# Kernel tuning notes

Hardware: AMD Instinct MI355X
Metric: run time of the kernel (lower is better)

## Reference

```python
import jax, jax.numpy as jnp
import numpy as np

LOG2 = 0.6931471805599453

def ssp(x):
    # ShiftedSoftplus: softplus(x) - log(2)
    return jax.nn.softplus(x) - jnp.asarray(LOG2, x.dtype)

def setup_inputs() -> dict:
    key = jax.random.key(0)
    ks = jax.random.split(key, 12)
    B, N, D, F, R, P = 1, 50000, 128, 128, 20, 1600000
    s = lambda fan_in: 1.0 / np.sqrt(fan_in)
    return {
        "x": jax.random.normal(ks[0], (B, N, D), jnp.float32),
        "f_ij": jax.random.uniform(ks[1], (P, R), jnp.float32),
        "idx_i": jax.random.randint(ks[2], (P,), 0, B * N),
        "idx_j": jax.random.randint(ks[3], (P,), 0, B * N),
        "rcut_ij": jax.random.uniform(ks[4], (P,), jnp.float32),
        "W_in": jax.random.uniform(ks[5], (F, D), jnp.float32, -s(D), s(D)),
        "b_in": jax.random.uniform(ks[6], (F,), jnp.float32, -s(D), s(D)),
        "W_filter": jax.random.uniform(ks[7], (F, R), jnp.float32, -s(R), s(R)),
        "b_filter": jax.random.uniform(ks[8], (F,), jnp.float32, -s(R), s(R)),
        "W_out": jax.random.uniform(ks[9], (D, F), jnp.float32, -s(F), s(F)),
        "b_out": jax.random.uniform(ks[10], (D,), jnp.float32, -s(F), s(F)),
    }

def reference(x, f_ij, idx_i, idx_j, rcut_ij, W_in, b_in, W_filter, b_filter, W_out, b_out):
    B, N, _ = x.shape
    # input_to_feature: Linear(nr_atom_basis -> nr_filters)
    h = jnp.einsum('bnd,fd->bnf', x, W_in) + b_in          # [B,N,F]
    h = h.reshape(B * N, -1)                                # [B*N,F]
    # filter network: Linear(nr_rbf -> nr_filters) + ShiftedSoftplus, scaled by cutoff
    Wij = ssp(jnp.einsum('pr,fr->pf', f_ij, W_filter) + b_filter) * rcut_ij[:, None]  # [P,F]
    # gather -> mul -> scatter_add
    x_ij = h[idx_j] * Wij                                   # [P,F]
    agg = jax.ops.segment_sum(x_ij, idx_i, num_segments=B * N)  # [B*N,F]
    # feature_to_output: Linear(nr_filters -> nr_atom_basis) + ShiftedSoftplus
    out = ssp(jnp.einsum('nf,df->nd', agg, W_out) + b_out)  # [B*N,D]
    return out.reshape(B, N, 128)
```

## Files before the change

### kernel.cpp

```cpp
#include <hip/hip_runtime.h>
#include <hip/hip_bf16.h>

static constexpr float kLog2 = 0.6931471805599453f;

__device__ __forceinline__ float sspf(float x) {
    return fmaxf(x, 0.0f) + __logf(1.0f + __expf(-fabsf(x))) - kLog2;
}

typedef __attribute__((ext_vector_type(8))) _Float16 half8;
typedef __attribute__((ext_vector_type(4))) _Float16 half4v;
typedef __attribute__((ext_vector_type(4))) float float4v;

template <bool ACT, typename OUT>
__device__ __forceinline__ void gemm_mfma_body(const float* __restrict__ A,
                                               const float* __restrict__ B,
                                               const float* __restrict__ bias,
                                               OUT* __restrict__ C, int M,
                                               int blockid) {
    constexpr int LDH = 136;
    __shared__ _Float16 Als[64 * LDH];
    __shared__ _Float16 Bls[128 * LDH];
    const int tid = threadIdx.x;
    const int rowbase = blockid * 64;
#pragma unroll
    for (int j = 0; j < 8; ++j) {
        int idx = j * 256 + tid;
        int r = idx >> 5, c4 = (idx & 31) << 2;
        int rg = rowbase + r;
        rg = rg < M ? rg : (M - 1);
        float4 v = *(const float4*)(A + (size_t)rg * 128 + c4);
        half4v hv = {(_Float16)v.x, (_Float16)v.y, (_Float16)v.z, (_Float16)v.w};
        *(half4v*)&Als[r * LDH + c4] = hv;
    }
#pragma unroll
    for (int j = 0; j < 16; ++j) {
        int idx = j * 256 + tid;
        int r = idx >> 5, c4 = (idx & 31) << 2;
        float4 v = *(const float4*)(B + (size_t)r * 128 + c4);
        half4v hv = {(_Float16)v.x, (_Float16)v.y, (_Float16)v.z, (_Float16)v.w};
        *(half4v*)&Bls[r * LDH + c4] = hv;
    }
    __syncthreads();

    const int wave = tid >> 6, lane = tid & 63;
    const int l15 = lane & 15, q = lane >> 4;
    float4v acc[8];
#pragma unroll
    for (int nt = 0; nt < 8; ++nt) acc[nt] = (float4v){0.f, 0.f, 0.f, 0.f};
    const int am = wave * 16 + l15;
#pragma unroll
    for (int kk = 0; kk < 4; ++kk) {
        half8 af = *(const half8*)&Als[am * LDH + kk * 32 + q * 8];
#pragma unroll
        for (int nt = 0; nt < 8; ++nt) {
            half8 bfv = *(const half8*)&Bls[(nt * 16 + l15) * LDH + kk * 32 + q * 8];
            acc[nt] = __builtin_amdgcn_mfma_f32_16x16x32_f16(af, bfv, acc[nt], 0, 0, 0);
        }
    }
#pragma unroll
    for (int nt = 0; nt < 8; ++nt) {
        int n = nt * 16 + l15;
        float bv = bias[n];
#pragma unroll
        for (int r = 0; r < 4; ++r) {
            int m = rowbase + wave * 16 + q * 4 + r;
            if (m < M) {
                float v = acc[nt][r] + bv;
                if (ACT) v = sspf(v);
                C[(size_t)m * 128 + n] = (OUT)v;
            }
        }
    }
}

__global__ __launch_bounds__(256) void gemm_in_count_kernel(
    const float* __restrict__ A, const float* __restrict__ B,
    const float* __restrict__ bias, _Float16* __restrict__ C, int M,
    const int* __restrict__ idx_i, int* __restrict__ counts, int P,
    int gemm_blocks) {
    if ((int)blockIdx.x < gemm_blocks) {
        gemm_mfma_body<false, _Float16>(A, B, bias, C, M, blockIdx.x);
    } else {
        const int nthr = (gridDim.x - gemm_blocks) * 256;
        for (int p = (blockIdx.x - gemm_blocks) * 256 + threadIdx.x; p < P;
             p += nthr)
            atomicAdd(&counts[idx_i[p]], 1);
    }
}

__global__ __launch_bounds__(256) void gemm_out_kernel(
    const float* __restrict__ A, const float* __restrict__ B,
    const float* __restrict__ bias, float* __restrict__ C, int M) {
    gemm_mfma_body<true, float>(A, B, bias, C, M, blockIdx.x);
}

__global__ __launch_bounds__(256) void alloc_starts_kernel(
    const int* __restrict__ counts, int* __restrict__ starts,
    int* __restrict__ cursor, int* __restrict__ gtot, int N) {
    __shared__ int s[256];
    __shared__ int base;
    const int t = threadIdx.x, g = blockIdx.x * 256 + t;
    const int c = g < N ? counts[g] : 0;
    s[t] = c;
    __syncthreads();
    for (int o = 1; o < 256; o <<= 1) {
        int v = t >= o ? s[t - o] : 0;
        __syncthreads();
        s[t] += v;
        __syncthreads();
    }
    if (t == 255) base = atomicAdd(gtot, s[255]);
    __syncthreads();
    const int excl = base + s[t] - c;
    if (g < N) {
        starts[g] = excl;
        cursor[g] = excl;
    }
}

template <bool EF>
__global__ __launch_bounds__(256) void fill_kernel(
    const int* __restrict__ idx_i, const int* __restrict__ idx_j,
    const float* __restrict__ rcut, const float* __restrict__ f_ij,
    int* __restrict__ cursor, _Float16* __restrict__ ef,
    int2* __restrict__ meta, int* __restrict__ pidx, int P) {
    int p = blockIdx.x * 256 + threadIdx.x;
    if (p >= P) return;
    const int i = idx_i[p];
    const int pos = atomicAdd(&cursor[i], 1);
    meta[pos] = make_int2(idx_j[p] << 7, __float_as_int(rcut[p]));
    if (EF) {
        const float* fr = f_ij + (size_t)p * 20;
        _Float16 hb[24];
#pragma unroll
        for (int r = 0; r < 20; r += 4) {
            float4 v = *(const float4*)(fr + r);
            hb[r] = (_Float16)v.x; hb[r + 1] = (_Float16)v.y;
            hb[r + 2] = (_Float16)v.z; hb[r + 3] = (_Float16)v.w;
        }
        hb[20] = (_Float16)1.0f; hb[21] = (_Float16)0.0f;
        hb[22] = (_Float16)0.0f; hb[23] = (_Float16)0.0f;
        _Float16* dst = ef + (size_t)pos * 24;
        *(half8*)dst = *(half8*)hb;
        *(half8*)(dst + 8) = *(half8*)(hb + 8);
        *(half8*)(dst + 16) = *(half8*)(hb + 16);
    } else {
        pidx[pos] = p;
    }
}

template <bool EF>
__global__ __launch_bounds__(256, 4) void gather_mfma_kernel(
    const _Float16* __restrict__ ef, const int2* __restrict__ meta,
    const int* __restrict__ pidx, const float* __restrict__ f_ij,
    const float* __restrict__ Wf, const float* __restrict__ bf,
    const _Float16* __restrict__ h16, const int* __restrict__ starts,
    const int* __restrict__ counts, float* __restrict__ agg, int N) {
    const int lane = threadIdx.x & 63;
    const int gwave = (blockIdx.x * 256 + threadIdx.x) >> 6;
    const int nwaves = (gridDim.x * 256) >> 6;
    const int l15 = lane & 15, q = lane >> 4;
    const int fh = gwave & 1;
    const int fbase = fh * 64;

    half8 wfr[4];
#pragma unroll
    for (int t = 0; t < 4; ++t) {
        const int n = fbase + t * 16 + l15;
        const float* wr = Wf + (size_t)n * 20;
        float v[8];
#pragma unroll
        for (int j = 0; j < 8; ++j) {
            int k = q * 8 + j;
            v[j] = (k < 20) ? wr[k] : ((k == 20) ? bf[n] : 0.0f);
        }
        wfr[t] = (half8){(_Float16)v[0], (_Float16)v[1], (_Float16)v[2],
                         (_Float16)v[3], (_Float16)v[4], (_Float16)v[5],
                         (_Float16)v[6], (_Float16)v[7]};
    }
    const float4v zero = {0.f, 0.f, 0.f, 0.f};
    const _Float16* hbase = h16 + fbase + q * 4;

    for (int u = gwave; u < 2 * N; u += nwaves) {
        const int i = u >> 1;
        const int s = __builtin_amdgcn_readfirstlane(starts[i]);
        const int cnt = __builtin_amdgcn_readfirstlane(counts[i]);
        const int e = s + cnt;
        float4v acc[4];
#pragma unroll
        for (int t = 0; t < 4; ++t) acc[t] = zero;

        if (cnt > 0) {
            int pos0 = min(s + l15, e - 1);
            int2 mt_c = meta[pos0];
            half8 bf_c = {};
            int p_c = 0;
            if (EF) {
                if (q < 3) bf_c = *(const half8*)(ef + (size_t)pos0 * 24 + q * 8);
            } else {
                p_c = pidx[pos0];
            }
            int2 mt_n = mt_c;
            half8 bf_n = bf_c;
            int p_n = p_c;
            if (s + 16 < e) {
                int pos1 = min(s + 16 + l15, e - 1);
                mt_n = meta[pos1];
                if (EF) {
                    if (q < 3) bf_n = *(const half8*)(ef + (size_t)pos1 * 24 + q * 8);
                } else {
                    p_n = pidx[pos1];
                }
            }
            half4v hv_c[4];
            {
                const _Float16* hp = hbase + mt_c.x;
#pragma unroll
                for (int t = 0; t < 4; ++t) hv_c[t] = *(const half4v*)(hp + t * 16);
            }

            for (int c = s; c < e; c += 16) {
                half4v hv_n[4];
                if (c + 16 < e) {
                    const _Float16* hp = hbase + mt_n.x;
#pragma unroll
                    for (int t = 0; t < 4; ++t) hv_n[t] = *(const half4v*)(hp + t * 16);
                }
                int2 mt_n2 = mt_n;
                half8 bf_n2 = bf_n;
                int p_n2 = p_n;
                if (c + 32 < e) {
                    int pos2 = min(c + 32 + l15, e - 1);
                    mt_n2 = meta[pos2];
                    if (EF) {
                        if (q < 3) bf_n2 = *(const half8*)(ef + (size_t)pos2 * 24 + q * 8);
                    } else {
                        p_n2 = pidx[pos2];
                    }
                }
                if (!EF) {
                    const float* fp = f_ij + (size_t)p_c * 20;
                    float b0 = 0.f, b1 = 0.f, b2 = 0.f, b3 = 0.f;
                    float b4 = 0.f, b5 = 0.f, b6 = 0.f, b7 = 0.f;
                    if (q <= 2) {
                        float4 a = *(const float4*)(fp + q * 8);
                        b0 = a.x; b1 = a.y; b2 = a.z; b3 = a.w;
                    }
                    if (q <= 1) {
                        float4 bb = *(const float4*)(fp + q * 8 + 4);
                        b4 = bb.x; b5 = bb.y; b6 = bb.z; b7 = bb.w;
                    }
                    if (q == 2) b4 = 1.0f;
                    bf_c = (half8){(_Float16)b0, (_Float16)b1, (_Float16)b2,
                                   (_Float16)b3, (_Float16)b4, (_Float16)b5,
                                   (_Float16)b6, (_Float16)b7};
                }
                const float rc = (c + l15 < e) ? __int_as_float(mt_c.y) : 0.0f;
#pragma unroll
                for (int t = 0; t < 4; ++t) {
                    float4v d = __builtin_amdgcn_mfma_f32_16x16x32_f16(
                        wfr[t], bf_c, zero, 0, 0, 0);
#pragma unroll
                    for (int r = 0; r < 4; ++r) {
                        float w = sspf(d[r]) * rc;
                        acc[t][r] = fmaf(w, (float)hv_c[t][r], acc[t][r]);
                    }
                }
                mt_c = mt_n; mt_n = mt_n2;
                bf_c = bf_n; bf_n = bf_n2;
                p_c = p_n;   p_n = p_n2;
#pragma unroll
                for (int t = 0; t < 4; ++t) hv_c[t] = hv_n[t];
            }
        }
#pragma unroll
        for (int m = 1; m <= 8; m <<= 1)
#pragma unroll
            for (int t = 0; t < 4; ++t)
#pragma unroll
                for (int r = 0; r < 4; ++r)
                    acc[t][r] += __shfl_xor(acc[t][r], m, 64);
        if (l15 == 0) {
#pragma unroll
            for (int t = 0; t < 4; ++t) {
                float4 o = {acc[t][0], acc[t][1], acc[t][2], acc[t][3]};
                *(float4*)(agg + (size_t)i * 128 + fbase + t * 16 + q * 4) = o;
            }
        }
    }
}

extern "C" void kernel_launch(void* const* d_in, const int* in_sizes, int n_in,
                              void* d_out, int out_size, void* d_ws, size_t ws_size,
                              hipStream_t stream) {
    const float* x     = (const float*)d_in[0];
    const float* f_ij  = (const float*)d_in[1];
    const int*   idx_i = (const int*)d_in[2];
    const int*   idx_j = (const int*)d_in[3];
    const float* rcut  = (const float*)d_in[4];
    const float* W_in  = (const float*)d_in[5];
    const float* b_in  = (const float*)d_in[6];
    const float* W_f   = (const float*)d_in[7];
    const float* b_f   = (const float*)d_in[8];
    const float* W_out = (const float*)d_in[9];
    const float* b_out = (const float*)d_in[10];

    const int N = in_sizes[0] / 128;
    const int P = in_sizes[2];

    char* ws = (char*)d_ws;
    size_t off = 0;
    auto alloc = [&](size_t bytes) {
        void* ptr = ws + off;
        off += (bytes + 15) & ~(size_t)15;
        return ptr;
    };
    int* counts  = (int*)alloc((size_t)N * 4 + 16);
    int* gtot    = counts + N;
    int* starts  = (int*)alloc((size_t)N * 4);
    int* cursor  = (int*)alloc((size_t)N * 4);
    _Float16* h16 = (_Float16*)alloc((size_t)N * 128 * 2);
    int2* meta   = (int2*)alloc((size_t)P * 8);
    size_t base_need = off;
    const bool use_ef = (base_need + (size_t)P * 24 * 2 + 64) <= ws_size;
    _Float16* ef = nullptr;
    int* pidx = nullptr;
    if (use_ef) ef = (_Float16*)alloc((size_t)P * 24 * 2 + 64);
    else        pidx = (int*)alloc((size_t)P * 4);

    float* agg = (float*)d_out;

    const int mblocks = (N + 63) / 64;
    const int cblocks = 768;
    const int NB = (N + 255) / 256;

    hipMemsetAsync(counts, 0, (size_t)N * 4 + 16, stream);
    gemm_in_count_kernel<<<mblocks + cblocks, 256, 0, stream>>>(
        x, W_in, b_in, h16, N, idx_i, counts, P, mblocks);
    alloc_starts_kernel<<<NB, 256, 0, stream>>>(counts, starts, cursor, gtot, N);
    if (use_ef) {
        fill_kernel<true><<<(P + 255) / 256, 256, 0, stream>>>(
            idx_i, idx_j, rcut, f_ij, cursor, ef, meta, pidx, P);
        gather_mfma_kernel<true><<<4096, 256, 0, stream>>>(
            ef, meta, pidx, f_ij, W_f, b_f, h16, starts, counts, agg, N);
    } else {
        fill_kernel<false><<<(P + 255) / 256, 256, 0, stream>>>(
            idx_i, idx_j, rcut, f_ij, cursor, ef, meta, pidx, P);
        gather_mfma_kernel<false><<<4096, 256, 0, stream>>>(
            ef, meta, pidx, f_ij, W_f, b_f, h16, starts, counts, agg, N);
    }
    gemm_out_kernel<<<mblocks, 256, 0, stream>>>(agg, W_out, b_out, (float*)d_out, N);
}
```

Measured before the change: 627.3 us.

## Precompute filter weights into CSR-ordered fp16 buffer, then lean gather-accumulate

Adds a filter_fill kernel that runs the filter MFMA and shifted softplus once per pair and writes fp16 W_ij rows into CSR order. A lean gather kernel then only loads W_ij and permuted h16 rows and accumulates them, instead of recomputing the filter inside the gather. Depending on workspace size, the filter is split into 1, 2 or 4 column chunks of 128/64/32 features. This removes MFMA and transcendental work from the latency-bound gather. In exchange it writes and re-reads a P×128 fp16 buffer, roughly 400 MB of extra traffic, and adds launches in the low-workspace modes.

```diff
diff --git a/kernel.cpp b/kernel.cpp
--- a/kernel.cpp
+++ b/kernel.cpp
@@ -11,7 +11,7 @@
 typedef __attribute__((ext_vector_type(4))) _Float16 half4v;
 typedef __attribute__((ext_vector_type(4))) float float4v;
 
-template <bool ACT, typename OUT>
+template <bool PERM, bool ACT, typename OUT>
 __device__ __forceinline__ void gemm_mfma_body(const float* __restrict__ A,
                                                const float* __restrict__ B,
                                                const float* __restrict__ bias,
@@ -61,25 +61,31 @@
     for (int nt = 0; nt < 8; ++nt) {
         int n = nt * 16 + l15;
         float bv = bias[n];
+        int pn = n;
+        if (PERM) {
+            pn = ((n >> 6) << 6) + (((n >> 2) & 3) << 4) + (((n >> 4) & 3) << 2) +
+                 (n & 3);
+        }
 #pragma unroll
         for (int r = 0; r < 4; ++r) {
             int m = rowbase + wave * 16 + q * 4 + r;
             if (m < M) {
                 float v = acc[nt][r] + bv;
                 if (ACT) v = sspf(v);
-                C[(size_t)m * 128 + n] = (OUT)v;
-            }
-        }
-    }
-}
-
+                C[(size_t)m * 128 + pn] = (OUT)v;
+            }
+        }
+    }
+}
+
+template <bool PERM>
 __global__ __launch_bounds__(256) void gemm_in_count_kernel(
     const float* __restrict__ A, const float* __restrict__ B,
     const float* __restrict__ bias, _Float16* __restrict__ C, int M,
     const int* __restrict__ idx_i, int* __restrict__ counts, int P,
     int gemm_blocks) {
     if ((int)blockIdx.x < gemm_blocks) {
-        gemm_mfma_body<false, _Float16>(A, B, bias, C, M, blockIdx.x);
+        gemm_mfma_body<PERM, false, _Float16>(A, B, bias, C, M, blockIdx.x);
     } else {
         const int nthr = (gridDim.x - gemm_blocks) * 256;
         for (int p = (blockIdx.x - gemm_blocks) * 256 + threadIdx.x; p < P;
@@ -91,7 +97,7 @@
 __global__ __launch_bounds__(256) void gemm_out_kernel(
     const float* __restrict__ A, const float* __restrict__ B,
     const float* __restrict__ bias, float* __restrict__ C, int M) {
-    gemm_mfma_body<true, float>(A, B, bias, C, M, blockIdx.x);
+    gemm_mfma_body<false, true, float>(A, B, bias, C, M, blockIdx.x);
 }
 
 __global__ __launch_bounds__(256) void alloc_starts_kernel(
@@ -115,6 +121,212 @@
     if (g < N) {
         starts[g] = excl;
         cursor[g] = excl;
+    }
+}
+
+
+template <int FT, bool ASSIGN>
+__global__ __launch_bounds__(256) void filter_fill_kernel(
+    const float* __restrict__ f_ij, const int* __restrict__ idx_i,
+    const int* __restrict__ idx_j, const float* __restrict__ rcut,
+    const float* __restrict__ Wf, const float* __restrict__ bfil,
+    int* __restrict__ cursor, int* __restrict__ meta, int* __restrict__ posof,
+    _Float16* __restrict__ wij, int P, int stride, int fb) {
+    const int lane = threadIdx.x & 63;
+    const int gw = (blockIdx.x * 256 + threadIdx.x) >> 6;
+    const int pb = gw * 16;
+    if (pb >= P) return;
+    const int l15 = lane & 15, q = lane >> 4;
+
+    half8 wfr[FT];
+#pragma unroll
+    for (int t = 0; t < FT; ++t) {
+        const int n = fb + t * 16 + l15;
+        const float* wr = Wf + (size_t)n * 20;
+        float v[8];
+#pragma unroll
+        for (int j = 0; j < 8; ++j) {
+            int k = q * 8 + j;
+            v[j] = (k < 20) ? wr[k] : ((k == 20) ? bfil[n] : 0.0f);
+        }
+        wfr[t] = (half8){(_Float16)v[0], (_Float16)v[1], (_Float16)v[2],
+                         (_Float16)v[3], (_Float16)v[4], (_Float16)v[5],
+                         (_Float16)v[6], (_Float16)v[7]};
+    }
+
+    const int p = pb + l15;
+    const bool pv = p < P;
+    const int pc = pv ? p : (P - 1);
+    const float rc = rcut[pc];
+
+    int pos;
+    if (ASSIGN) {
+        int pos0 = 0;
+        if (q == 0 && pv) {
+            pos0 = atomicAdd(&cursor[idx_i[p]], 1);
+            meta[pos0] = idx_j[p] << 7;
+            posof[p] = pos0;
+        }
+        pos = __shfl(pos0, l15, 64);
+    } else {
+        pos = posof[pc];
+    }
+
+    const float* fp = f_ij + (size_t)pc * 20;
+    float b0 = 0.f, b1 = 0.f, b2 = 0.f, b3 = 0.f;
+    float b4 = 0.f, b5 = 0.f, b6 = 0.f, b7 = 0.f;
+    if (q <= 2) {
+        float4 a = *(const float4*)(fp + q * 8);
+        b0 = a.x; b1 = a.y; b2 = a.z; b3 = a.w;
+    }
+    if (q <= 1) {
+        float4 bb = *(const float4*)(fp + q * 8 + 4);
+        b4 = bb.x; b5 = bb.y; b6 = bb.z; b7 = bb.w;
+    }
+    if (q == 2) b4 = 1.0f;
+    const half8 bfc = (half8){(_Float16)b0, (_Float16)b1, (_Float16)b2,
+                              (_Float16)b3, (_Float16)b4, (_Float16)b5,
+                              (_Float16)b6, (_Float16)b7};
+
+    const float4v zero = {0.f, 0.f, 0.f, 0.f};
+    const float rcln2 = rc * 0.69314718f;
+    _Float16 wst[FT * 4];
+#pragma unroll
+    for (int t = 0; t < FT; ++t) {
+        float4v d = __builtin_amdgcn_mfma_f32_16x16x32_f16(wfr[t], bfc, zero, 0, 0, 0);
+#pragma unroll
+        for (int r = 0; r < 4; ++r) {
+            float x = d[r];
+            float mx = fmaxf(x, 0.0f);
+            float e2 = exp2f(-fabsf(x) * 1.44269504f);
+            float lg = log2f(1.0f + e2);
+            float w = fmaf(lg, rcln2, fmaf(mx, rc, -rcln2));
+            wst[t * 4 + r] = (_Float16)w;
+        }
+    }
+    if (pv) {
+        _Float16* wb = wij + (size_t)pos * stride;
+        if (FT == 8) {
+            *(half8*)(wb + q * 16) = *(half8*)&wst[0];
+            *(half8*)(wb + q * 16 + 8) = *(half8*)&wst[8];
+            *(half8*)(wb + 64 + q * 16) = *(half8*)&wst[16];
+            *(half8*)(wb + 64 + q * 16 + 8) = *(half8*)&wst[24];
+        } else if (FT == 4) {
+            *(half8*)(wb + q * 16) = *(half8*)&wst[0];
+            *(half8*)(wb + q * 16 + 8) = *(half8*)&wst[8];
+        } else {
+            *(half8*)(wb + q * 8) = *(half8*)&wst[0];
+        }
+    }
+}
+
+template <int GT>
+__global__ __launch_bounds__(256) void gather_lean_kernel(
+    const _Float16* __restrict__ wij, const int* __restrict__ meta,
+    const _Float16* __restrict__ h16, const int* __restrict__ starts,
+    const int* __restrict__ counts, float* __restrict__ agg, int units,
+    int stride, int fb_fixed, int split) {
+    constexpr int NH = GT / 2;
+    const int lane = threadIdx.x & 63;
+    const int gwave = (blockIdx.x * 256 + threadIdx.x) >> 6;
+    const int nwaves = (gridDim.x * 256) >> 6;
+    const int l15 = lane & 15, q = lane >> 4;
+    const half8 hzero = {};
+
+    for (int u = gwave; u < units; u += nwaves) {
+        int i, fbw, woff;
+        if (split) {
+            i = u >> 1;
+            fbw = (u & 1) << 6;
+            woff = fbw + (q << 4);
+        } else {
+            i = u;
+            fbw = fb_fixed;
+            woff = q * (GT * 4);
+        }
+        const int hoff = ((fbw >> 6) << 6) + (q << 4) + (((fbw >> 4) & 3) << 2);
+        const int s = __builtin_amdgcn_readfirstlane(starts[i]);
+        const int cnt = __builtin_amdgcn_readfirstlane(counts[i]);
+        const int e = s + cnt;
+        float4v acc[GT];
+#pragma unroll
+        for (int t = 0; t < GT; ++t) acc[t] = (float4v){0.f, 0.f, 0.f, 0.f};
+
+        if (cnt > 0) {
+            int pos_c = min(s + l15, e - 1);
+            bool vl_c = (s + l15) < e;
+            int jb_c = meta[pos_c];
+            half8 wv_c[NH], hv_c[NH];
+            {
+                const _Float16* wp = wij + (size_t)pos_c * stride + woff;
+                const _Float16* hp = h16 + jb_c + hoff;
+#pragma unroll
+                for (int h = 0; h < NH; ++h) {
+                    wv_c[h] = *(const half8*)(wp + h * 8);
+                    hv_c[h] = *(const half8*)(hp + h * 8);
+                }
+            }
+            int pos_n = pos_c, jb_n = jb_c;
+            bool vl_n = false;
+            if (s + 16 < e) {
+                pos_n = min(s + 16 + l15, e - 1);
+                jb_n = meta[pos_n];
+                vl_n = (s + 16 + l15) < e;
+            }
+            for (int c = s; c < e; c += 16) {
+                half8 wv_n[NH], hv_n[NH];
+                if (c + 16 < e) {
+                    const _Float16* wp = wij + (size_t)pos_n * stride + woff;
+                    const _Float16* hp = h16 + jb_n + hoff;
+#pragma unroll
+                    for (int h = 0; h < NH; ++h) {
+                        wv_n[h] = *(const half8*)(wp + h * 8);
+                        hv_n[h] = *(const half8*)(hp + h * 8);
+                    }
+                }
+                int pos_n2 = pos_n, jb_n2 = jb_n;
+                bool vl_n2 = vl_n;
+                if (c + 32 < e) {
+                    pos_n2 = min(c + 32 + l15, e - 1);
+                    jb_n2 = meta[pos_n2];
+                    vl_n2 = (c + 32 + l15) < e;
+                }
+                if (!vl_c) {
+#pragma unroll
+                    for (int h = 0; h < NH; ++h) wv_c[h] = hzero;
+                }
+#pragma unroll
+                for (int h = 0; h < NH; ++h) {
+#pragma unroll
+                    for (int j = 0; j < 8; ++j) {
+                        int t = (h * 8 + j) >> 2, r = j & 3;
+                        acc[t][r] = fmaf((float)wv_c[h][j], (float)hv_c[h][j],
+                                         acc[t][r]);
+                    }
+                }
+#pragma unroll
+                for (int h = 0; h < NH; ++h) {
+                    wv_c[h] = wv_n[h];
+                    hv_c[h] = hv_n[h];
+                }
+                vl_c = vl_n; vl_n = vl_n2;
+                pos_n = pos_n2; jb_n = jb_n2;
+            }
+        }
+#pragma unroll
+        for (int m = 1; m <= 8; m <<= 1)
+#pragma unroll
+            for (int t = 0; t < GT; ++t)
+#pragma unroll
+                for (int r = 0; r < 4; ++r)
+                    acc[t][r] += __shfl_xor(acc[t][r], m, 64);
+        if (l15 == 0) {
+#pragma unroll
+            for (int t = 0; t < GT; ++t) {
+                float4 o = {acc[t][0], acc[t][1], acc[t][2], acc[t][3]};
+                *(float4*)(agg + (size_t)i * 128 + fbw + t * 16 + q * 4) = o;
+            }
+        }
     }
 }
 
@@ -255,6 +467,8 @@
                                    (_Float16)b3, (_Float16)b4, (_Float16)b5,
                                    (_Float16)b6, (_Float16)b7};
                 }
+                const int jb = mt_c.x;
+                (void)jb;
                 const float rc = (c + l15 < e) ? __int_as_float(mt_c.y) : 0.0f;
 #pragma unroll
                 for (int t = 0; t < 4; ++t) {
@@ -308,6 +522,24 @@
     const int N = in_sizes[0] / 128;
     const int P = in_sizes[2];
 
+    const int mblocks = (N + 63) / 64;
+    const int cblocks = 768;
+    const int NB = (N + 255) / 256;
+    float* agg = (float*)d_out;
+
+    auto pad16 = [](size_t b) { return (b + 15) & ~(size_t)15; };
+
+    size_t base_new = pad16((size_t)N * 4 + 16) + pad16((size_t)N * 4) +
+                      pad16((size_t)N * 4) + pad16((size_t)N * 128 * 2) +
+                      pad16((size_t)P * 4) + pad16((size_t)P * 4);
+    auto wij_bytes = [&](int stride) { return pad16((size_t)P * stride * 2 + 64); };
+
+    int mode;
+    if (base_new + wij_bytes(128) <= ws_size) mode = 0;
+    else if (base_new + wij_bytes(64) <= ws_size) mode = 1;
+    else if (base_new + wij_bytes(32) <= ws_size) mode = 2;
+    else mode = 3;
+
     char* ws = (char*)d_ws;
     size_t off = 0;
     auto alloc = [&](size_t bytes) {
@@ -315,12 +547,74 @@
         off += (bytes + 15) & ~(size_t)15;
         return ptr;
     };
+
+    if (mode != 3) {
+        int* counts  = (int*)alloc((size_t)N * 4 + 16);
+        int* gtot    = counts + N;
+        int* starts  = (int*)alloc((size_t)N * 4);
+        int* cursor  = (int*)alloc((size_t)N * 4);
+        _Float16* h16 = (_Float16*)alloc((size_t)N * 128 * 2);
+        int* meta    = (int*)alloc((size_t)P * 4);
+        int* posof   = (int*)alloc((size_t)P * 4);
+        const int stride = (mode == 0) ? 128 : (mode == 1 ? 64 : 32);
+        _Float16* wij = (_Float16*)alloc((size_t)P * stride * 2 + 64);
+
+        hipMemsetAsync(counts, 0, (size_t)N * 4 + 16, stream);
+        gemm_in_count_kernel<true><<<mblocks + cblocks, 256, 0, stream>>>(
+            x, W_in, b_in, h16, N, idx_i, counts, P, mblocks);
+        alloc_starts_kernel<<<NB, 256, 0, stream>>>(counts, starts, cursor, gtot, N);
+
+        const int fblocks = (P + 63) / 64;
+        if (mode == 0) {
+            filter_fill_kernel<8, true><<<fblocks, 256, 0, stream>>>(
+                f_ij, idx_i, idx_j, rcut, W_f, b_f, cursor, meta, posof, wij, P,
+                128, 0);
+            gather_lean_kernel<4><<<4096, 256, 0, stream>>>(
+                wij, meta, h16, starts, counts, agg, 2 * N, 128, 0, 1);
+        } else if (mode == 1) {
+            filter_fill_kernel<4, true><<<fblocks, 256, 0, stream>>>(
+                f_ij, idx_i, idx_j, rcut, W_f, b_f, cursor, meta, posof, wij, P,
+                64, 0);
+            gather_lean_kernel<4><<<4096, 256, 0, stream>>>(
+                wij, meta, h16, starts, counts, agg, N, 64, 0, 0);
+            filter_fill_kernel<4, false><<<fblocks, 256, 0, stream>>>(
+                f_ij, idx_i, idx_j, rcut, W_f, b_f, cursor, meta, posof, wij, P,
+                64, 64);
+            gather_lean_kernel<4><<<4096, 256, 0, stream>>>(
+                wij, meta, h16, starts, counts, agg, N, 64, 64, 0);
+        } else {
+            filter_fill_kernel<2, true><<<fblocks, 256, 0, stream>>>(
+                f_ij, idx_i, idx_j, rcut, W_f, b_f, cursor, meta, posof, wij, P,
+                32, 0);
+            gather_lean_kernel<2><<<4096, 256, 0, stream>>>(
+                wij, meta, h16, starts, counts, agg, N, 32, 0, 0);
+            filter_fill_kernel<2, false><<<fblocks, 256, 0, stream>>>(
+                f_ij, idx_i, idx_j, rcut, W_f, b_f, cursor, meta, posof, wij, P,
+                32, 32);
+            gather_lean_kernel<2><<<4096, 256, 0, stream>>>(
+                wij, meta, h16, starts, counts, agg, N, 32, 32, 0);
+            filter_fill_kernel<2, false><<<fblocks, 256, 0, stream>>>(
+                f_ij, idx_i, idx_j, rcut, W_f, b_f, cursor, meta, posof, wij, P,
+                32, 64);
+            gather_lean_kernel<2><<<4096, 256, 0, stream>>>(
+                wij, meta, h16, starts, counts, agg, N, 32, 64, 0);
+            filter_fill_kernel<2, false><<<fblocks, 256, 0, stream>>>(
+                f_ij, idx_i, idx_j, rcut, W_f, b_f, cursor, meta, posof, wij, P,
+                32, 96);
+            gather_lean_kernel<2><<<4096, 256, 0, stream>>>(
+                wij, meta, h16, starts, counts, agg, N, 32, 96, 0);
+        }
+        gemm_out_kernel<<<mblocks, 256, 0, stream>>>(agg, W_out, b_out,
+                                                     (float*)d_out, N);
+        return;
+    }
+
     int* counts  = (int*)alloc((size_t)N * 4 + 16);
     int* gtot    = counts + N;
     int* starts  = (int*)alloc((size_t)N * 4);
     int* cursor  = (int*)alloc((size_t)N * 4);
     _Float16* h16 = (_Float16*)alloc((size_t)N * 128 * 2);
-    int2* meta   = (int2*)alloc((size_t)P * 8);
+    int2* meta2  = (int2*)alloc((size_t)P * 8);
     size_t base_need = off;
     const bool use_ef = (base_need + (size_t)P * 24 * 2 + 64) <= ws_size;
     _Float16* ef = nullptr;
@@ -328,26 +622,20 @@
     if (use_ef) ef = (_Float16*)alloc((size_t)P * 24 * 2 + 64);
     else        pidx = (int*)alloc((size_t)P * 4);
 
-    float* agg = (float*)d_out;
-
-    const int mblocks = (N + 63) / 64;
-    const int cblocks = 768;
-    const int NB = (N + 255) / 256;
-
     hipMemsetAsync(counts, 0, (size_t)N * 4 + 16, stream);
-    gemm_in_count_kernel<<<mblocks + cblocks, 256, 0, stream>>>(
+    gemm_in_count_kernel<false><<<mblocks + cblocks, 256, 0, stream>>>(
         x, W_in, b_in, h16, N, idx_i, counts, P, mblocks);
     alloc_starts_kernel<<<NB, 256, 0, stream>>>(counts, starts, cursor, gtot, N);
     if (use_ef) {
         fill_kernel<true><<<(P + 255) / 256, 256, 0, stream>>>(
-            idx_i, idx_j, rcut, f_ij, cursor, ef, meta, pidx, P);
+            idx_i, idx_j, rcut, f_ij, cursor, ef, meta2, pidx, P);
         gather_mfma_kernel<true><<<4096, 256, 0, stream>>>(
-            ef, meta, pidx, f_ij, W_f, b_f, h16, starts, counts, agg, N);
+            ef, meta2, pidx, f_ij, W_f, b_f, h16, starts, counts, agg, N);
     } else {
         fill_kernel<false><<<(P + 255) / 256, 256, 0, stream>>>(
-            idx_i, idx_j, rcut, f_ij, cursor, ef, meta, pidx, P);
+            idx_i, idx_j, rcut, f_ij, cursor, ef, meta2, pidx, P);
         gather_mfma_kernel<false><<<4096, 256, 0, stream>>>(
-            ef, meta, pidx, f_ij, W_f, b_f, h16, starts, counts, agg, N);
+            ef, meta2, pidx, f_ij, W_f, b_f, h16, starts, counts, agg, N);
     }
     gemm_out_kernel<<<mblocks, 256, 0, stream>>>(agg, W_out, b_out, (float*)d_out, N);
 }
```

New measurement: 1.023 ms. +63.1%, slower.

## Permute h16 columns so one wave gathers full 128-feature rows per atom

Applied to the files above, without the earlier changes.

The input GEMM now writes h16 with a permuted column order, so each lane can load contiguous half8 chunks that match the MFMA output layout of the filter network. The gather kernel processes all 128 filters per atom in a single wave instead of splitting them across two waves. This halves the metadata and edge-feature loads and the filter MFMA input setup per edge. In exchange it doubles the register footprint (8 filter fragments, 8 accumulators), so the occupancy hint of 4 is removed and occupancy and latency hiding may drop.

```diff
diff --git a/kernel.cpp b/kernel.cpp
--- a/kernel.cpp
+++ b/kernel.cpp
@@ -11,7 +11,12 @@
 typedef __attribute__((ext_vector_type(4))) _Float16 half4v;
 typedef __attribute__((ext_vector_type(4))) float float4v;
 
-template <bool ACT, typename OUT>
+__device__ __forceinline__ int hperm(int n) {
+    return ((n >> 6) << 6) | (((n >> 5) & 1) << 5) | (((n >> 2) & 3) << 3) |
+           (((n >> 4) & 1) << 2) | (n & 3);
+}
+
+template <bool PERM, bool ACT, typename OUT>
 __device__ __forceinline__ void gemm_mfma_body(const float* __restrict__ A,
                                                const float* __restrict__ B,
                                                const float* __restrict__ bias,
@@ -61,13 +66,14 @@
     for (int nt = 0; nt < 8; ++nt) {
         int n = nt * 16 + l15;
         float bv = bias[n];
+        const int pn = PERM ? hperm(n) : n;
 #pragma unroll
         for (int r = 0; r < 4; ++r) {
             int m = rowbase + wave * 16 + q * 4 + r;
             if (m < M) {
                 float v = acc[nt][r] + bv;
                 if (ACT) v = sspf(v);
-                C[(size_t)m * 128 + n] = (OUT)v;
+                C[(size_t)m * 128 + pn] = (OUT)v;
             }
         }
     }
@@ -79,7 +85,7 @@
     const int* __restrict__ idx_i, int* __restrict__ counts, int P,
     int gemm_blocks) {
     if ((int)blockIdx.x < gemm_blocks) {
-        gemm_mfma_body<false, _Float16>(A, B, bias, C, M, blockIdx.x);
+        gemm_mfma_body<true, false, _Float16>(A, B, bias, C, M, blockIdx.x);
     } else {
         const int nthr = (gridDim.x - gemm_blocks) * 256;
         for (int p = (blockIdx.x - gemm_blocks) * 256 + threadIdx.x; p < P;
@@ -91,7 +97,7 @@
 __global__ __launch_bounds__(256) void gemm_out_kernel(
     const float* __restrict__ A, const float* __restrict__ B,
     const float* __restrict__ bias, float* __restrict__ C, int M) {
-    gemm_mfma_body<true, float>(A, B, bias, C, M, blockIdx.x);
+    gemm_mfma_body<false, true, float>(A, B, bias, C, M, blockIdx.x);
 }
 
 __global__ __launch_bounds__(256) void alloc_starts_kernel(
@@ -150,7 +156,7 @@
 }
 
 template <bool EF>
-__global__ __launch_bounds__(256, 4) void gather_mfma_kernel(
+__global__ __launch_bounds__(256) void gather_mfma_kernel(
     const _Float16* __restrict__ ef, const int2* __restrict__ meta,
     const int* __restrict__ pidx, const float* __restrict__ f_ij,
     const float* __restrict__ Wf, const float* __restrict__ bf,
@@ -160,35 +166,30 @@
     const int gwave = (blockIdx.x * 256 + threadIdx.x) >> 6;
     const int nwaves = (gridDim.x * 256) >> 6;
     const int l15 = lane & 15, q = lane >> 4;
-    const int fh = gwave & 1;
-    const int fbase = fh * 64;
-
-    half8 wfr[4];
-#pragma unroll
-    for (int t = 0; t < 4; ++t) {
-        const int n = fbase + t * 16 + l15;
-        const float* wr = Wf + (size_t)n * 20;
+
+    half8 wfr[8];
+#pragma unroll
+    for (int t = 0; t < 8; ++t) {
+        const float* wr = Wf + (size_t)(t * 16 + l15) * 20;
         float v[8];
 #pragma unroll
         for (int j = 0; j < 8; ++j) {
             int k = q * 8 + j;
-            v[j] = (k < 20) ? wr[k] : ((k == 20) ? bf[n] : 0.0f);
+            v[j] = (k < 20) ? wr[k] : ((k == 20) ? bf[t * 16 + l15] : 0.0f);
         }
         wfr[t] = (half8){(_Float16)v[0], (_Float16)v[1], (_Float16)v[2],
                          (_Float16)v[3], (_Float16)v[4], (_Float16)v[5],
                          (_Float16)v[6], (_Float16)v[7]};
     }
     const float4v zero = {0.f, 0.f, 0.f, 0.f};
-    const _Float16* hbase = h16 + fbase + q * 4;
-
-    for (int u = gwave; u < 2 * N; u += nwaves) {
-        const int i = u >> 1;
+
+    for (int i = gwave; i < N; i += nwaves) {
         const int s = __builtin_amdgcn_readfirstlane(starts[i]);
         const int cnt = __builtin_amdgcn_readfirstlane(counts[i]);
         const int e = s + cnt;
-        float4v acc[4];
-#pragma unroll
-        for (int t = 0; t < 4; ++t) acc[t] = zero;
+        float4v acc[8];
+#pragma unroll
+        for (int t = 0; t < 8; ++t) acc[t] = zero;
 
         if (cnt > 0) {
             int pos0 = min(s + l15, e - 1);
@@ -212,25 +213,27 @@
                     p_n = pidx[pos1];
                 }
             }
-            half4v hv_c[4];
+            half8 hv_c[4];
             {
-                const _Float16* hp = hbase + mt_c.x;
-#pragma unroll
-                for (int t = 0; t < 4; ++t) hv_c[t] = *(const half4v*)(hp + t * 16);
-            }
-
-            for (int c = s; c < e; c += 16) {
-                half4v hv_n[4];
-                if (c + 16 < e) {
-                    const _Float16* hp = hbase + mt_n.x;
-#pragma unroll
-                    for (int t = 0; t < 4; ++t) hv_n[t] = *(const half4v*)(hp + t * 16);
+                const _Float16* hp = h16 + mt_c.x + q * 8;
+#pragma unroll
+                for (int c4 = 0; c4 < 4; ++c4)
+                    hv_c[c4] = *(const half8*)(hp + c4 * 32);
+            }
+
+            for (int c0 = s; c0 < e; c0 += 16) {
+                half8 hv_n[4];
+                if (c0 + 16 < e) {
+                    const _Float16* hp = h16 + mt_n.x + q * 8;
+#pragma unroll
+                    for (int c4 = 0; c4 < 4; ++c4)
+                        hv_n[c4] = *(const half8*)(hp + c4 * 32);
                 }
                 int2 mt_n2 = mt_n;
                 half8 bf_n2 = bf_n;
                 int p_n2 = p_n;
-                if (c + 32 < e) {
-                    int pos2 = min(c + 32 + l15, e - 1);
+                if (c0 + 32 < e) {
+                    int pos2 = min(c0 + 32 + l15, e - 1);
                     mt_n2 = meta[pos2];
                     if (EF) {
                         if (q < 3) bf_n2 = *(const half8*)(ef + (size_t)pos2 * 24 + q * 8);
@@ -255,36 +258,37 @@
                                    (_Float16)b3, (_Float16)b4, (_Float16)b5,
                                    (_Float16)b6, (_Float16)b7};
                 }
-                const float rc = (c + l15 < e) ? __int_as_float(mt_c.y) : 0.0f;
-#pragma unroll
-                for (int t = 0; t < 4; ++t) {
+                const float rc = (c0 + l15 < e) ? __int_as_float(mt_c.y) : 0.0f;
+#pragma unroll
+                for (int t = 0; t < 8; ++t) {
                     float4v d = __builtin_amdgcn_mfma_f32_16x16x32_f16(
                         wfr[t], bf_c, zero, 0, 0, 0);
+                    const int hc = t >> 1, hb = (t & 1) * 4;
 #pragma unroll
                     for (int r = 0; r < 4; ++r) {
                         float w = sspf(d[r]) * rc;
-                        acc[t][r] = fmaf(w, (float)hv_c[t][r], acc[t][r]);
+                        acc[t][r] = fmaf(w, (float)hv_c[hc][hb + r], acc[t][r]);
                     }
                 }
                 mt_c = mt_n; mt_n = mt_n2;
                 bf_c = bf_n; bf_n = bf_n2;
                 p_c = p_n;   p_n = p_n2;
 #pragma unroll
-                for (int t = 0; t < 4; ++t) hv_c[t] = hv_n[t];
+                for (int c4 = 0; c4 < 4; ++c4) hv_c[c4] = hv_n[c4];
             }
         }
 #pragma unroll
         for (int m = 1; m <= 8; m <<= 1)
 #pragma unroll
-            for (int t = 0; t < 4; ++t)
+            for (int t = 0; t < 8; ++t)
 #pragma unroll
                 for (int r = 0; r < 4; ++r)
                     acc[t][r] += __shfl_xor(acc[t][r], m, 64);
         if (l15 == 0) {
 #pragma unroll
-            for (int t = 0; t < 4; ++t) {
+            for (int t = 0; t < 8; ++t) {
                 float4 o = {acc[t][0], acc[t][1], acc[t][2], acc[t][3]};
-                *(float4*)(agg + (size_t)i * 128 + fbase + t * 16 + q * 4) = o;
+                *(float4*)(agg + (size_t)i * 128 + t * 16 + q * 4) = o;
             }
         }
     }
```

Result: slower. 695.2 us (+10.8%).

## Drop packed fp16 edge-feature buffer; gather f_ij directly and permute h16 columns

Applied to the files above, without the earlier changes.

The fill kernel no longer converts and scatters f_ij into a sorted fp16 buffer. It only writes a 16-byte meta record (idx_j offset, rcut, original edge index). The gather kernel reads f_ij rows directly through the stored edge index, prefetching one chunk ahead. The input GEMM writes h16 with a column permutation so each lane loads two half8 vectors instead of four half4 vectors. This removes the 1.6M×48-byte ef write and read in exchange for random reads of f_ij in the gather and a larger meta record, and it drops the h prefetch pipelining.

```diff
diff --git a/kernel.cpp b/kernel.cpp
--- a/kernel.cpp
+++ b/kernel.cpp
@@ -11,7 +11,12 @@
 typedef __attribute__((ext_vector_type(4))) _Float16 half4v;
 typedef __attribute__((ext_vector_type(4))) float float4v;
 
-template <bool ACT, typename OUT>
+__device__ __forceinline__ int hperm(int n) {
+    return ((n >> 6) << 6) | (((n >> 5) & 1) << 5) | (((n >> 2) & 3) << 3) |
+           (((n >> 4) & 1) << 2) | (n & 3);
+}
+
+template <bool PERM, bool ACT, typename OUT>
 __device__ __forceinline__ void gemm_mfma_body(const float* __restrict__ A,
                                                const float* __restrict__ B,
                                                const float* __restrict__ bias,
@@ -61,13 +66,14 @@
     for (int nt = 0; nt < 8; ++nt) {
         int n = nt * 16 + l15;
         float bv = bias[n];
+        const int pn = PERM ? hperm(n) : n;
 #pragma unroll
         for (int r = 0; r < 4; ++r) {
             int m = rowbase + wave * 16 + q * 4 + r;
             if (m < M) {
                 float v = acc[nt][r] + bv;
                 if (ACT) v = sspf(v);
-                C[(size_t)m * 128 + n] = (OUT)v;
+                C[(size_t)m * 128 + pn] = (OUT)v;
             }
         }
     }
@@ -79,7 +85,7 @@
     const int* __restrict__ idx_i, int* __restrict__ counts, int P,
     int gemm_blocks) {
     if ((int)blockIdx.x < gemm_blocks) {
-        gemm_mfma_body<false, _Float16>(A, B, bias, C, M, blockIdx.x);
+        gemm_mfma_body<true, false, _Float16>(A, B, bias, C, M, blockIdx.x);
     } else {
         const int nthr = (gridDim.x - gemm_blocks) * 256;
         for (int p = (blockIdx.x - gemm_blocks) * 256 + threadIdx.x; p < P;
@@ -91,7 +97,7 @@
 __global__ __launch_bounds__(256) void gemm_out_kernel(
     const float* __restrict__ A, const float* __restrict__ B,
     const float* __restrict__ bias, float* __restrict__ C, int M) {
-    gemm_mfma_body<true, float>(A, B, bias, C, M, blockIdx.x);
+    gemm_mfma_body<false, true, float>(A, B, bias, C, M, blockIdx.x);
 }
 
 __global__ __launch_bounds__(256) void alloc_starts_kernel(
@@ -118,41 +124,18 @@
     }
 }
 
-template <bool EF>
-__global__ __launch_bounds__(256) void fill_kernel(
+__global__ __launch_bounds__(256) void fill16_kernel(
     const int* __restrict__ idx_i, const int* __restrict__ idx_j,
-    const float* __restrict__ rcut, const float* __restrict__ f_ij,
-    int* __restrict__ cursor, _Float16* __restrict__ ef,
-    int2* __restrict__ meta, int* __restrict__ pidx, int P) {
+    const float* __restrict__ rcut, int* __restrict__ cursor,
+    int4* __restrict__ meta, int P) {
     int p = blockIdx.x * 256 + threadIdx.x;
     if (p >= P) return;
-    const int i = idx_i[p];
-    const int pos = atomicAdd(&cursor[i], 1);
-    meta[pos] = make_int2(idx_j[p] << 7, __float_as_int(rcut[p]));
-    if (EF) {
-        const float* fr = f_ij + (size_t)p * 20;
-        _Float16 hb[24];
-#pragma unroll
-        for (int r = 0; r < 20; r += 4) {
-            float4 v = *(const float4*)(fr + r);
-            hb[r] = (_Float16)v.x; hb[r + 1] = (_Float16)v.y;
-            hb[r + 2] = (_Float16)v.z; hb[r + 3] = (_Float16)v.w;
-        }
-        hb[20] = (_Float16)1.0f; hb[21] = (_Float16)0.0f;
-        hb[22] = (_Float16)0.0f; hb[23] = (_Float16)0.0f;
-        _Float16* dst = ef + (size_t)pos * 24;
-        *(half8*)dst = *(half8*)hb;
-        *(half8*)(dst + 8) = *(half8*)(hb + 8);
-        *(half8*)(dst + 16) = *(half8*)(hb + 16);
-    } else {
-        pidx[pos] = p;
-    }
-}
-
-template <bool EF>
-__global__ __launch_bounds__(256, 4) void gather_mfma_kernel(
-    const _Float16* __restrict__ ef, const int2* __restrict__ meta,
-    const int* __restrict__ pidx, const float* __restrict__ f_ij,
+    const int pos = atomicAdd(&cursor[idx_i[p]], 1);
+    meta[pos] = make_int4(idx_j[p] << 7, __float_as_int(rcut[p]), p, 0);
+}
+
+__global__ __launch_bounds__(256) void gather_direct_kernel(
+    const int4* __restrict__ meta, const float* __restrict__ f_ij,
     const float* __restrict__ Wf, const float* __restrict__ bf,
     const _Float16* __restrict__ h16, const int* __restrict__ starts,
     const int* __restrict__ counts, float* __restrict__ agg, int N) {
@@ -179,7 +162,7 @@
                          (_Float16)v[6], (_Float16)v[7]};
     }
     const float4v zero = {0.f, 0.f, 0.f, 0.f};
-    const _Float16* hbase = h16 + fbase + q * 4;
+    const _Float16* hws = h16 + fbase + q * 8;
 
     for (int u = gwave; u < 2 * N; u += nwaves) {
         const int i = u >> 1;
@@ -191,86 +174,53 @@
         for (int t = 0; t < 4; ++t) acc[t] = zero;
 
         if (cnt > 0) {
-            int pos0 = min(s + l15, e - 1);
-            int2 mt_c = meta[pos0];
-            half8 bf_c = {};
-            int p_c = 0;
-            if (EF) {
-                if (q < 3) bf_c = *(const half8*)(ef + (size_t)pos0 * 24 + q * 8);
-            } else {
-                p_c = pidx[pos0];
-            }
-            int2 mt_n = mt_c;
-            half8 bf_n = bf_c;
-            int p_n = p_c;
-            if (s + 16 < e) {
-                int pos1 = min(s + 16 + l15, e - 1);
-                mt_n = meta[pos1];
-                if (EF) {
-                    if (q < 3) bf_n = *(const half8*)(ef + (size_t)pos1 * 24 + q * 8);
-                } else {
-                    p_n = pidx[pos1];
-                }
-            }
-            half4v hv_c[4];
+            int4 mt_c = meta[min(s + l15, e - 1)];
+            int4 mt_n = (s + 16 < e) ? meta[min(s + 16 + l15, e - 1)] : mt_c;
+            float4 fa_c = {0, 0, 0, 0}, fb_c = {0, 0, 0, 0};
+            float4 fa_p = {0, 0, 0, 0}, fb_p = {0, 0, 0, 0};
             {
-                const _Float16* hp = hbase + mt_c.x;
-#pragma unroll
-                for (int t = 0; t < 4; ++t) hv_c[t] = *(const half4v*)(hp + t * 16);
-            }
-
-            for (int c = s; c < e; c += 16) {
-                half4v hv_n[4];
-                if (c + 16 < e) {
-                    const _Float16* hp = hbase + mt_n.x;
-#pragma unroll
-                    for (int t = 0; t < 4; ++t) hv_n[t] = *(const half4v*)(hp + t * 16);
-                }
-                int2 mt_n2 = mt_n;
-                half8 bf_n2 = bf_n;
-                int p_n2 = p_n;
-                if (c + 32 < e) {
-                    int pos2 = min(c + 32 + l15, e - 1);
-                    mt_n2 = meta[pos2];
-                    if (EF) {
-                        if (q < 3) bf_n2 = *(const half8*)(ef + (size_t)pos2 * 24 + q * 8);
-                    } else {
-                        p_n2 = pidx[pos2];
-                    }
-                }
-                if (!EF) {
-                    const float* fp = f_ij + (size_t)p_c * 20;
-                    float b0 = 0.f, b1 = 0.f, b2 = 0.f, b3 = 0.f;
-                    float b4 = 0.f, b5 = 0.f, b6 = 0.f, b7 = 0.f;
-                    if (q <= 2) {
-                        float4 a = *(const float4*)(fp + q * 8);
-                        b0 = a.x; b1 = a.y; b2 = a.z; b3 = a.w;
-                    }
-                    if (q <= 1) {
-                        float4 bb = *(const float4*)(fp + q * 8 + 4);
-                        b4 = bb.x; b5 = bb.y; b6 = bb.z; b7 = bb.w;
-                    }
-                    if (q == 2) b4 = 1.0f;
-                    bf_c = (half8){(_Float16)b0, (_Float16)b1, (_Float16)b2,
-                                   (_Float16)b3, (_Float16)b4, (_Float16)b5,
-                                   (_Float16)b6, (_Float16)b7};
-                }
-                const float rc = (c + l15 < e) ? __int_as_float(mt_c.y) : 0.0f;
+                const float* fp = f_ij + (size_t)mt_c.z * 20;
+                if (q <= 2) fa_c = *(const float4*)(fp + q * 8);
+                if (q <= 1) fb_c = *(const float4*)(fp + q * 8 + 4);
+                const float* fp2 = f_ij + (size_t)mt_n.z * 20;
+                if (q <= 2) fa_p = *(const float4*)(fp2 + q * 8);
+                if (q <= 1) fb_p = *(const float4*)(fp2 + q * 8 + 4);
+            }
+
+            for (int c0 = s; c0 < e; c0 += 16) {
+                const _Float16* hp = hws + mt_c.x;
+                half8 hv0 = *(const half8*)hp;
+                half8 hv1 = *(const half8*)(hp + 32);
+                int4 mt_n2 = mt_n;
+                if (c0 + 32 < e) mt_n2 = meta[min(c0 + 32 + l15, e - 1)];
+                float b0 = 0.f, b1 = 0.f, b2 = 0.f, b3 = 0.f;
+                float b4 = 0.f, b5 = 0.f, b6 = 0.f, b7 = 0.f;
+                if (q <= 2) { b0 = fa_c.x; b1 = fa_c.y; b2 = fa_c.z; b3 = fa_c.w; }
+                if (q <= 1) { b4 = fb_c.x; b5 = fb_c.y; b6 = fb_c.z; b7 = fb_c.w; }
+                if (q == 2) b4 = 1.0f;
+                const half8 bfc = (half8){(_Float16)b0, (_Float16)b1, (_Float16)b2,
+                                          (_Float16)b3, (_Float16)b4, (_Float16)b5,
+                                          (_Float16)b6, (_Float16)b7};
+                const float rc = (c0 + l15 < e) ? __int_as_float(mt_c.y) : 0.0f;
 #pragma unroll
                 for (int t = 0; t < 4; ++t) {
                     float4v d = __builtin_amdgcn_mfma_f32_16x16x32_f16(
-                        wfr[t], bf_c, zero, 0, 0, 0);
+                        wfr[t], bfc, zero, 0, 0, 0);
+                    const half8& hv = (t < 2) ? hv0 : hv1;
+                    const int hb = (t & 1) * 4;
 #pragma unroll
                     for (int r = 0; r < 4; ++r) {
                         float w = sspf(d[r]) * rc;
-                        acc[t][r] = fmaf(w, (float)hv_c[t][r], acc[t][r]);
+                        acc[t][r] = fmaf(w, (float)hv[hb + r], acc[t][r]);
                     }
                 }
                 mt_c = mt_n; mt_n = mt_n2;
-                bf_c = bf_n; bf_n = bf_n2;
-                p_c = p_n;   p_n = p_n2;
-#pragma unroll
-                for (int t = 0; t < 4; ++t) hv_c[t] = hv_n[t];
+                fa_c = fa_p; fb_c = fb_p;
+                if (c0 + 32 < e) {
+                    const float* fp = f_ij + (size_t)mt_n.z * 20;
+                    if (q <= 2) fa_p = *(const float4*)(fp + q * 8);
+                    if (q <= 1) fb_p = *(const float4*)(fp + q * 8 + 4);
+                }
             }
         }
 #pragma unroll
@@ -320,13 +270,7 @@
     int* starts  = (int*)alloc((size_t)N * 4);
     int* cursor  = (int*)alloc((size_t)N * 4);
     _Float16* h16 = (_Float16*)alloc((size_t)N * 128 * 2);
-    int2* meta   = (int2*)alloc((size_t)P * 8);
-    size_t base_need = off;
-    const bool use_ef = (base_need + (size_t)P * 24 * 2 + 64) <= ws_size;
-    _Float16* ef = nullptr;
-    int* pidx = nullptr;
-    if (use_ef) ef = (_Float16*)alloc((size_t)P * 24 * 2 + 64);
-    else        pidx = (int*)alloc((size_t)P * 4);
+    int4* meta   = (int4*)alloc((size_t)P * 16);
 
     float* agg = (float*)d_out;
 
@@ -338,16 +282,9 @@
     gemm_in_count_kernel<<<mblocks + cblocks, 256, 0, stream>>>(
         x, W_in, b_in, h16, N, idx_i, counts, P, mblocks);
     alloc_starts_kernel<<<NB, 256, 0, stream>>>(counts, starts, cursor, gtot, N);
-    if (use_ef) {
-        fill_kernel<true><<<(P + 255) / 256, 256, 0, stream>>>(
-            idx_i, idx_j, rcut, f_ij, cursor, ef, meta, pidx, P);
-        gather_mfma_kernel<true><<<4096, 256, 0, stream>>>(
-            ef, meta, pidx, f_ij, W_f, b_f, h16, starts, counts, agg, N);
-    } else {
-        fill_kernel<false><<<(P + 255) / 256, 256, 0, stream>>>(
-            idx_i, idx_j, rcut, f_ij, cursor, ef, meta, pidx, P);
-        gather_mfma_kernel<false><<<4096, 256, 0, stream>>>(
-            ef, meta, pidx, f_ij, W_f, b_f, h16, starts, counts, agg, N);
-    }
+    fill16_kernel<<<(P + 255) / 256, 256, 0, stream>>>(
+        idx_i, idx_j, rcut, cursor, meta, P);
+    gather_direct_kernel<<<4096, 256, 0, stream>>>(
+        meta, f_ij, W_f, b_f, h16, starts, counts, agg, N);
     gemm_out_kernel<<<mblocks, 256, 0, stream>>>(agg, W_out, b_out, (float*)d_out, N);
 }
```

After: 677.1 us. +7.9%, slower.
